# Kernel tuning notes

Hardware: AMD Instinct MI355X
Metric: run time of the kernel (lower is better)

The kernel has to match this reference:

```python
import jax, jax.numpy as jnp
import numpy as np

FP8_E4M3_MAX = 448.0

def setup_inputs() -> dict:
    key = jax.random.key(0)
    k1, k2, k3 = jax.random.split(key, 3)
    B, S, D_IN, D_OUT = 2, 4096, 2048, 8192
    x = jax.random.normal(k1, (B, S, D_IN), dtype=jnp.float32)
    # Xavier-uniform init for weight [out, in]
    limit = np.sqrt(6.0 / (D_IN + D_OUT)).astype(np.float32)
    weight = jax.random.uniform(k2, (D_OUT, D_IN), dtype=jnp.float32, minval=-limit, maxval=limit)
    bias = jax.random.normal(k3, (D_OUT,), dtype=jnp.float32) * 0.02
    return {"x": x, "weight": weight, "bias": bias}

def reference(x, weight, bias):
    # Dynamic amax-based scales (most_recent algo); treated as constants (torch uses .item())
    w_scale = jax.lax.stop_gradient(jnp.max(jnp.abs(weight)) / FP8_E4M3_MAX)
    x_scale = jax.lax.stop_gradient(jnp.max(jnp.abs(x)) / FP8_E4M3_MAX)
    # Quantize: divide by scale, cast (bf16 stands in for fp8 e4m3, as in the fallback branch)
    w_q = (weight / w_scale).astype(jnp.bfloat16)
    x_q = (x / x_scale).astype(jnp.bfloat16)
    # Matmul in quantized domain, then rescale
    out = jnp.einsum('bsd,od->bso', x_q, w_q)  # bf16 accumulate per fallback semantics
    out = out.astype(jnp.float32) * (w_scale * x_scale)
    out = out + bias
    return out.astype(x.dtype)
```

## Files before the change

### kernel.cpp

```cpp
#include <hip/hip_runtime.h>
#include <hip/hip_bf16.h>

#define M_DIM 8192
#define N_DIM 8192
#define K_DIM 2048
#define BM 128
#define BN 128
#define BK 32

typedef __attribute__((ext_vector_type(8))) short bf16x8;
typedef __attribute__((ext_vector_type(4))) float floatx4;

__device__ inline void gload_lds16(const void* g, void* l) {
  __builtin_amdgcn_global_load_lds(
      (const __attribute__((address_space(1))) unsigned int*)g,
      (__attribute__((address_space(3))) unsigned int*)l, 16, 0, 0);
}

__device__ inline short f2bf(float f) {
  __hip_bfloat16 h = __float2bfloat16(f);
  return *(short*)&h;
}

__device__ inline float round_bf16(float f) {
  __hip_bfloat16 h = __float2bfloat16(f);
  return __bfloat162float(h);
}

__global__ __launch_bounds__(256) void amax_kernel(const float* __restrict__ src,
                                                   int n,
                                                   unsigned int* __restrict__ out_bits) {
  int tid = threadIdx.x;
  int start = (blockIdx.x * 256 + tid) * 4;
  int stride = gridDim.x * 256 * 4;
  float m = 0.0f;
  for (int i = start; i < n; i += stride) {
    float4 v = *(const float4*)(src + i);
    m = fmaxf(m, fmaxf(fmaxf(fabsf(v.x), fabsf(v.y)), fmaxf(fabsf(v.z), fabsf(v.w))));
  }
  for (int off = 32; off > 0; off >>= 1) m = fmaxf(m, __shfl_down(m, off));
  __shared__ float red[4];
  if ((tid & 63) == 0) red[tid >> 6] = m;
  __syncthreads();
  if (tid == 0) {
    m = fmaxf(fmaxf(red[0], red[1]), fmaxf(red[2], red[3]));
    atomicMax(out_bits, __float_as_uint(m));
  }
}

__global__ __launch_bounds__(256) void quant_kernel(const float* __restrict__ src,
                                                    short* __restrict__ dst,
                                                    const unsigned int* __restrict__ amax_bits) {
  float scale = __uint_as_float(*amax_bits) / 448.0f;
  int idx = (blockIdx.x * 256 + threadIdx.x) * 8;
  float4 v0 = *(const float4*)(src + idx);
  float4 v1 = *(const float4*)(src + idx + 4);
  bf16x8 o;
  o[0] = f2bf(v0.x / scale);
  o[1] = f2bf(v0.y / scale);
  o[2] = f2bf(v0.z / scale);
  o[3] = f2bf(v0.w / scale);
  o[4] = f2bf(v1.x / scale);
  o[5] = f2bf(v1.y / scale);
  o[6] = f2bf(v1.z / scale);
  o[7] = f2bf(v1.w / scale);
  *(bf16x8*)(dst + idx) = o;
}

__global__ __launch_bounds__(256, 2) void gemm_kernel(
    const short* __restrict__ A,
    const short* __restrict__ B,
    const float* __restrict__ bias,
    const unsigned int* __restrict__ amax_bits,
    float* __restrict__ C) {
  __shared__ short As[BM * BK];
  __shared__ short Bs[BN * BK];

  const int tid = threadIdx.x;
  const int lane = tid & 63;
  const int waveId = tid >> 6;
  const int waveM = waveId >> 1;
  const int waveN = waveId & 1;
  const int m0 = blockIdx.y * BM;
  const int n0 = blockIdx.x * BN;

  const int r0 = tid >> 2;
  const int q0 = tid & 3;
  const short* aSrc0 = A + (long)(m0 + r0) * K_DIM + q0 * 8;
  const short* aSrc1 = A + (long)(m0 + r0 + 64) * K_DIM + q0 * 8;
  const short* bSrc0 = B + (long)(n0 + r0) * K_DIM + q0 * 8;
  const short* bSrc1 = B + (long)(n0 + r0 + 64) * K_DIM + q0 * 8;
  short* aDst0 = As + tid * 8;
  short* aDst1 = As + (tid + 256) * 8;
  short* bDst0 = Bs + tid * 8;
  short* bDst1 = Bs + (tid + 256) * 8;

  floatx4 acc[4][4] = {};

  const int am = waveM * 64 + (lane & 15);
  const int bn = waveN * 64 + (lane & 15);
  const int ak = (lane >> 4) * 8;

  for (int kt = 0; kt < K_DIM / BK; ++kt) {
    const int ko = kt * BK;
    gload_lds16(aSrc0 + ko, aDst0);
    gload_lds16(aSrc1 + ko, aDst1);
    gload_lds16(bSrc0 + ko, bDst0);
    gload_lds16(bSrc1 + ko, bDst1);
    __syncthreads();

    bf16x8 af[4], bfr[4];
#pragma unroll
    for (int i = 0; i < 4; ++i)
      af[i] = *(const bf16x8*)(As + (am + i * 16) * BK + ak);
#pragma unroll
    for (int j = 0; j < 4; ++j)
      bfr[j] = *(const bf16x8*)(Bs + (bn + j * 16) * BK + ak);

#pragma unroll
    for (int i = 0; i < 4; ++i)
#pragma unroll
      for (int j = 0; j < 4; ++j)
        acc[i][j] = __builtin_amdgcn_mfma_f32_16x16x32_bf16(af[i], bfr[j], acc[i][j], 0, 0, 0);

    __syncthreads();
  }

  const float sx = __uint_as_float(amax_bits[0]) / 448.0f;
  const float sw = __uint_as_float(amax_bits[1]) / 448.0f;
  const float s = sx * sw;
  const int col = lane & 15;
  const int rq = (lane >> 4) * 4;
#pragma unroll
  for (int j = 0; j < 4; ++j) {
    const int n = n0 + waveN * 64 + j * 16 + col;
    const float bv = bias[n];
#pragma unroll
    for (int i = 0; i < 4; ++i) {
      const int mBase = m0 + waveM * 64 + i * 16 + rq;
#pragma unroll
      for (int r = 0; r < 4; ++r) {
        float v = round_bf16(acc[i][j][r]);
        C[(long)(mBase + r) * N_DIM + n] = v * s + bv;
      }
    }
  }
}

extern "C" void kernel_launch(void* const* d_in, const int* in_sizes, int n_in,
                              void* d_out, int out_size, void* d_ws, size_t ws_size,
                              hipStream_t stream) {
  const float* x = (const float*)d_in[0];
  const float* w = (const float*)d_in[1];
  const float* bias = (const float*)d_in[2];
  float* out = (float*)d_out;

  unsigned int* bits = (unsigned int*)d_ws;
  short* xq = (short*)((char*)d_ws + 256);
  short* wq = (short*)((char*)d_ws + 256 + (size_t)M_DIM * K_DIM * sizeof(short));

  hipMemsetAsync(d_ws, 0, 64, stream);

  amax_kernel<<<1024, 256, 0, stream>>>(x, M_DIM * K_DIM, bits + 0);
  amax_kernel<<<1024, 256, 0, stream>>>(w, N_DIM * K_DIM, bits + 1);

  quant_kernel<<<M_DIM * K_DIM / (256 * 8), 256, 0, stream>>>(x, xq, bits + 0);
  quant_kernel<<<N_DIM * K_DIM / (256 * 8), 256, 0, stream>>>(w, wq, bits + 1);

  gemm_kernel<<<dim3(N_DIM / BN, M_DIM / BM), 256, 0, stream>>>(xq, wq, bias, bits, out);
}
```

Baseline: 675.7 us.

## Merge amax/quant launches for x and w and XOR-swizzle GEMM LDS layout

The two amax launches become one grid that handles both x and w, and the two quantize launches are merged the same way, which removes kernel launches and the idle tail between them. The GEMM applies an XOR swizzle to the k-chunk index. Each thread's global source column is permuted at load time and the MFMA fragment read offset is permuted to match, so the LDS bf16x8 reads spread across banks instead of conflicting. The data placed in LDS stays consistent with the read pattern, but the swizzle has to match exactly for the results to remain correct.

```diff
diff --git a/kernel.cpp b/kernel.cpp
--- a/kernel.cpp
+++ b/kernel.cpp
@@ -27,12 +27,17 @@
   return __bfloat162float(h);
 }
 
-__global__ __launch_bounds__(256) void amax_kernel(const float* __restrict__ src,
-                                                   int n,
-                                                   unsigned int* __restrict__ out_bits) {
+__global__ __launch_bounds__(256) void amax2_kernel(const float* __restrict__ x,
+                                                    const float* __restrict__ w,
+                                                    int n,
+                                                    unsigned int* __restrict__ bits) {
+  int b = blockIdx.x;
+  const float* src;
+  unsigned int* ob;
+  if (b < 1024) { src = x; ob = bits + 0; } else { src = w; ob = bits + 1; b -= 1024; }
   int tid = threadIdx.x;
-  int start = (blockIdx.x * 256 + tid) * 4;
-  int stride = gridDim.x * 256 * 4;
+  int start = (b * 256 + tid) * 4;
+  const int stride = 1024 * 256 * 4;
   float m = 0.0f;
   for (int i = start; i < n; i += stride) {
     float4 v = *(const float4*)(src + i);
@@ -44,15 +49,23 @@
   __syncthreads();
   if (tid == 0) {
     m = fmaxf(fmaxf(red[0], red[1]), fmaxf(red[2], red[3]));
-    atomicMax(out_bits, __float_as_uint(m));
+    atomicMax(ob, __float_as_uint(m));
   }
 }
 
-__global__ __launch_bounds__(256) void quant_kernel(const float* __restrict__ src,
-                                                    short* __restrict__ dst,
-                                                    const unsigned int* __restrict__ amax_bits) {
-  float scale = __uint_as_float(*amax_bits) / 448.0f;
-  int idx = (blockIdx.x * 256 + threadIdx.x) * 8;
+__global__ __launch_bounds__(256) void quant2_kernel(const float* __restrict__ x,
+                                                     const float* __restrict__ w,
+                                                     short* __restrict__ xq,
+                                                     short* __restrict__ wq,
+                                                     const unsigned int* __restrict__ bits) {
+  int b = blockIdx.x;
+  const float* src;
+  short* dst;
+  const unsigned int* ab;
+  if (b < 8192) { src = x; dst = xq; ab = bits + 0; }
+  else          { src = w; dst = wq; ab = bits + 1; b -= 8192; }
+  float scale = __uint_as_float(*ab) / 448.0f;
+  int idx = (b * 256 + threadIdx.x) * 8;
   float4 v0 = *(const float4*)(src + idx);
   float4 v1 = *(const float4*)(src + idx + 4);
   bf16x8 o;
@@ -85,7 +98,7 @@
   const int n0 = blockIdx.x * BN;
 
   const int r0 = tid >> 2;
-  const int q0 = tid & 3;
+  const int q0 = (tid & 3) ^ ((tid >> 3) & 3);
   const short* aSrc0 = A + (long)(m0 + r0) * K_DIM + q0 * 8;
   const short* aSrc1 = A + (long)(m0 + r0 + 64) * K_DIM + q0 * 8;
   const short* bSrc0 = B + (long)(n0 + r0) * K_DIM + q0 * 8;
@@ -99,7 +112,7 @@
 
   const int am = waveM * 64 + (lane & 15);
   const int bn = waveN * 64 + (lane & 15);
-  const int ak = (lane >> 4) * 8;
+  const int ak = ((lane >> 4) ^ ((lane >> 1) & 3)) * 8;
 
   for (int kt = 0; kt < K_DIM / BK; ++kt) {
     const int ko = kt * BK;
@@ -161,11 +174,7 @@
 
   hipMemsetAsync(d_ws, 0, 64, stream);
 
-  amax_kernel<<<1024, 256, 0, stream>>>(x, M_DIM * K_DIM, bits + 0);
-  amax_kernel<<<1024, 256, 0, stream>>>(w, N_DIM * K_DIM, bits + 1);
-
-  quant_kernel<<<M_DIM * K_DIM / (256 * 8), 256, 0, stream>>>(x, xq, bits + 0);
-  quant_kernel<<<N_DIM * K_DIM / (256 * 8), 256, 0, stream>>>(w, wq, bits + 1);
-
+  amax2_kernel<<<2048, 256, 0, stream>>>(x, w, M_DIM * K_DIM, bits);
+  quant2_kernel<<<16384, 256, 0, stream>>>(x, w, xq, wq, bits);
   gemm_kernel<<<dim3(N_DIM / BN, M_DIM / BM), 256, 0, stream>>>(xq, wq, bias, bits, out);
 }
```

Measured after the change: 667.4 us. About the same (-1.2%).
